# Kernel optimization log

Hardware: AMD Instinct MI355X
Metric: run time of the kernel (lower is better)

Reference implementation:

```python
import jax, jax.numpy as jnp
import numpy as np

L, D, H, EXP = 4, 512, 8, 4
HD = D // H
DFF = D * EXP
B, S = 8, 1024
LN_EPS = 1e-3  # keras LayerNormalization default epsilon


def _glorot(key, shape):
    fan_in, fan_out = shape[-2], shape[-1]
    lim = np.sqrt(6.0 / (fan_in + fan_out))
    return jax.random.uniform(key, shape, jnp.float32, -lim, lim)


def setup_inputs() -> dict:
    key = jax.random.key(0)
    ks = jax.random.split(key, 12)
    x = jax.random.normal(ks[0], (B, S, D), jnp.float32)
    # sequence mask from random lengths (mimics tf.sequence_mask(row_lengths))
    lengths = jax.random.randint(ks[1], (B,), S // 2, S + 1)
    mask = (jnp.arange(S)[None, :] < lengths[:, None])  # [B,S] bool
    inp = {
        'x': x, 'mask': mask,
        'Wq': _glorot(ks[2], (L, D, D)),
        'Wk': _glorot(ks[3], (L, D, D)),
        'Wv': _glorot(ks[4], (L, D, D)),
        'Wo': _glorot(ks[5], (L, D, D)),
        'ln1_g': jnp.ones((L, D), jnp.float32),
        'ln1_b': jnp.zeros((L, D), jnp.float32),
        'ln2_g': jnp.ones((L, D), jnp.float32),
        'ln2_b': jnp.zeros((L, D), jnp.float32),
        'W1': _glorot(ks[6], (L, D, DFF)),
        'b1': jnp.zeros((L, DFF), jnp.float32),
        'W2': _glorot(ks[7], (L, DFF, D)),
        'b2': jnp.zeros((L, D), jnp.float32),
    }
    return inp


def _layernorm(x, g, b):
    mu = jnp.mean(x, axis=-1, keepdims=True)
    var = jnp.mean(jnp.square(x - mu), axis=-1, keepdims=True)
    return (x - mu) * jax.lax.rsqrt(var + LN_EPS) * g + b


def _pos_encoding(s, d):
    # matches the source: sin/cos halves with inv freq 10000**(2j/d), j<d/2
    half = d // 2
    p = jnp.arange(s, dtype=jnp.float32)[:, None]          # [S,1]
    inv = 10000.0 ** (2.0 * jnp.arange(half, dtype=jnp.float32) / d)  # [half]
    ang = p / inv[None, :]                                 # [S,half]
    return jnp.concatenate([jnp.sin(ang), jnp.cos(ang)], axis=1)  # [S,D]


def _forward(x, mask, Wq, Wk, Wv, Wo, ln1_g, ln1_b, ln2_g, ln2_b, W1, b1, W2, b2):
    b, s, d = x.shape
    x = x + _pos_encoding(s, d)
    key_mask = mask[:, None, None, :]  # [B,1,1,Sk]
    scale = 1.0 / jnp.sqrt(jnp.float32(HD))
    for l in range(L):
        h = _layernorm(x, ln1_g[l], ln1_b[l])
        q = (h @ Wq[l]).reshape(b, s, H, HD).transpose(0, 2, 1, 3)  # bhsd
        k = (h @ Wk[l]).reshape(b, s, H, HD).transpose(0, 2, 1, 3)
        v = (h @ Wv[l]).reshape(b, s, H, HD).transpose(0, 2, 1, 3)
        scores = jnp.einsum('bhqd,bhkd->bhqk', q, k) * scale
        scores = jnp.where(key_mask, scores, -1e9)
        attn = jax.nn.softmax(scores, axis=-1)
        o = jnp.einsum('bhqk,bhkd->bhqd', attn, v)
        o = o.transpose(0, 2, 1, 3).reshape(b, s, d) @ Wo[l]
        x = x + o  # dropout rate 0 / inference -> identity
        h = _layernorm(x, ln2_g[l], ln2_b[l])
        f = jax.nn.relu(h @ W1[l] + b1[l]) @ W2[l] + b2[l]
        x = x + f
    return x


def reference(x, mask, Wq, Wk, Wv, Wo, ln1_g, ln1_b, ln2_g, ln2_b, W1, b1, W2, b2):
    return _forward(x, mask, Wq, Wk, Wv, Wo, ln1_g, ln1_b, ln2_g, ln2_b, W1, b1, W2, b2)
```

## Files before the change

### kernel.cpp

```cpp
#include <hip/hip_runtime.h>
#include <math.h>

#define NB 8
#define SEQ 1024
#define DM 512
#define NH 8
#define HDIM 64
#define DFF 2048
#define NLAYER 4
#define NTOK (NB * SEQ)
#define QKVD 1536

typedef __attribute__((ext_vector_type(8))) short bf16x8;
typedef __attribute__((ext_vector_type(4))) float f32x4;

__device__ __forceinline__ ushort f2bf(float f) {
    union { float f; unsigned u; } v; v.f = f;
    unsigned r = (v.u + 0x7FFF + ((v.u >> 16) & 1)) >> 16;
    return (ushort)r;
}

__device__ __forceinline__ void async16(const void* g, void* l) {
    __builtin_amdgcn_global_load_lds(
        (const __attribute__((address_space(1))) unsigned int*)g,
        (__attribute__((address_space(3))) unsigned int*)l, 16, 0, 0);
}

__global__ __launch_bounds__(256) void add_pos_kernel(const float* __restrict__ x,
                                                      float* __restrict__ out) {
    int idx4 = blockIdx.x * blockDim.x + threadIdx.x;
    int base = idx4 * 4;
    int d = base & (DM - 1);
    int s = (base >> 9) & (SEQ - 1);
    float4 v = *(const float4*)&x[base];
    float r[4] = {v.x, v.y, v.z, v.w};
#pragma unroll
    for (int i = 0; i < 4; i++) {
        int dd = d + i;
        float pe;
        if (dd < 256) {
            float inv = powf(10000.0f, 2.0f * (float)dd / 512.0f);
            pe = sinf((float)s / inv);
        } else {
            float inv = powf(10000.0f, 2.0f * (float)(dd - 256) / 512.0f);
            pe = cosf((float)s / inv);
        }
        r[i] += pe;
    }
    *(float4*)&out[base] = make_float4(r[0], r[1], r[2], r[3]);
}

__global__ __launch_bounds__(256) void wtrans_kernel(const float* __restrict__ src,
                                                     ushort* __restrict__ dst,
                                                     int K, int N, int rowOff,
                                                     int layerStride) {
    __shared__ float tile[32][36];
    int l = blockIdx.z;
    int kb = blockIdx.y * 32, nb = blockIdx.x * 32;
    const float* s = src + (size_t)l * K * N;
    ushort* d = dst + (size_t)l * layerStride;
    int r = threadIdx.x >> 3, c4 = (threadIdx.x & 7) * 4;
    float4 v = *(const float4*)&s[(size_t)(kb + r) * N + nb + c4];
    *(float4*)&tile[r][c4] = v;
    __syncthreads();
    ushort4 o;
    o.x = f2bf(tile[c4 + 0][r]);
    o.y = f2bf(tile[c4 + 1][r]);
    o.z = f2bf(tile[c4 + 2][r]);
    o.w = f2bf(tile[c4 + 3][r]);
    *(ushort4*)&d[(size_t)(rowOff + nb + r) * K + kb + c4] = o;
}

__global__ __launch_bounds__(256) void ln_kernel(const float* __restrict__ x,
                                                 const float* __restrict__ g,
                                                 const float* __restrict__ bta,
                                                 ushort* __restrict__ out) {
    int w = threadIdx.x >> 6;
    int lane = threadIdx.x & 63;
    size_t row = (size_t)blockIdx.x * 4 + w;
    const float* xr = x + row * DM;
    float4 v0 = *(const float4*)&xr[lane * 4];
    float4 v1 = *(const float4*)&xr[256 + lane * 4];
    float sum = v0.x + v0.y + v0.z + v0.w + v1.x + v1.y + v1.z + v1.w;
#pragma unroll
    for (int off = 32; off > 0; off >>= 1) sum += __shfl_xor(sum, off, 64);
    float mu = sum * (1.0f / 512.0f);
    float d0[8] = {v0.x - mu, v0.y - mu, v0.z - mu, v0.w - mu,
                   v1.x - mu, v1.y - mu, v1.z - mu, v1.w - mu};
    float sq = 0.0f;
#pragma unroll
    for (int i = 0; i < 8; i++) sq = fmaf(d0[i], d0[i], sq);
#pragma unroll
    for (int off = 32; off > 0; off >>= 1) sq += __shfl_xor(sq, off, 64);
    float rs = rsqrtf(sq * (1.0f / 512.0f) + 1e-3f);
    float4 g0 = *(const float4*)&g[lane * 4];
    float4 g1 = *(const float4*)&g[256 + lane * 4];
    float4 b0 = *(const float4*)&bta[lane * 4];
    float4 b1 = *(const float4*)&bta[256 + lane * 4];
    ushort* orow = out + row * DM;
    ushort4 o0, o1;
    o0.x = f2bf(fmaf(d0[0] * rs, g0.x, b0.x));
    o0.y = f2bf(fmaf(d0[1] * rs, g0.y, b0.y));
    o0.z = f2bf(fmaf(d0[2] * rs, g0.z, b0.z));
    o0.w = f2bf(fmaf(d0[3] * rs, g0.w, b0.w));
    o1.x = f2bf(fmaf(d0[4] * rs, g1.x, b1.x));
    o1.y = f2bf(fmaf(d0[5] * rs, g1.y, b1.y));
    o1.z = f2bf(fmaf(d0[6] * rs, g1.z, b1.z));
    o1.w = f2bf(fmaf(d0[7] * rs, g1.w, b1.w));
    *(ushort4*)&orow[lane * 4] = o0;
    *(ushort4*)&orow[256 + lane * 4] = o1;
}

template <int BM, int BN, int KH, int MODE>
__global__ __launch_bounds__(512) void gemm_bf16(const ushort* __restrict__ A,
                                                 const ushort* __restrict__ Bt,
                                                 const float* __restrict__ bias,
                                                 void* __restrict__ Cv,
                                                 void* __restrict__ aux,
                                                 int M, int N, int K) {
    static_assert(BM % 64 == 0 && BN % 64 == 0, "tile multiple of 64");
    constexpr int FM = BM / 64;
    constexpr int FN = BN / 32;
    __shared__ __align__(16) ushort As[2][KH * BM * 32];
    __shared__ __align__(16) ushort Bs[2][KH * BN * 32];
    const int tid = threadIdx.x;
    const int lane = tid & 63;
    const int w = tid >> 6;

    const int nx = gridDim.x;
    int wg = blockIdx.y * nx + blockIdx.x;
    int xcd = wg & 7;
    int t0 = wg >> 3;
    int bx = t0 % nx;
    int by = (t0 / nx) * 8 + xcd;
    const int m0 = by * BM, n0 = bx * BN;

    const int wm = (w >> 1) * (BM / 4);
    const int wn = (w & 1) * (BN / 2);
    const int fm = lane & 15, fq = lane >> 4;

    f32x4 acc[FM][FN] = {};

    auto stage = [&](int buf, int kt) {
#pragma unroll
        for (int hf = 0; hf < KH; hf++) {
            constexpr int CA = BM * 4;
            if constexpr (CA >= 512) {
#pragma unroll
                for (int u = 0; u < CA / 512; u++) {
                    int chunk = u * 512 + tid;
                    int row = chunk >> 2, c = chunk & 3;
                    async16(&A[(size_t)(m0 + row) * K + kt + hf * 32 + c * 8],
                            (char*)As[buf] + hf * BM * 64 + chunk * 16);
                }
            } else {
                if (tid < CA) {
                    int chunk = tid;
                    int row = chunk >> 2, c = chunk & 3;
                    async16(&A[(size_t)(m0 + row) * K + kt + hf * 32 + c * 8],
                            (char*)As[buf] + hf * BM * 64 + chunk * 16);
                }
            }
            constexpr int CB = BN * 4;
            if constexpr (CB >= 512) {
#pragma unroll
                for (int u = 0; u < CB / 512; u++) {
                    int chunk = u * 512 + tid;
                    int row = chunk >> 2, c = chunk & 3;
                    async16(&Bt[(size_t)(n0 + row) * K + kt + hf * 32 + c * 8],
                            (char*)Bs[buf] + hf * BN * 64 + chunk * 16);
                }
            } else {
                if (tid < CB) {
                    int chunk = tid;
                    int row = chunk >> 2, c = chunk & 3;
                    async16(&Bt[(size_t)(n0 + row) * K + kt + hf * 32 + c * 8],
                            (char*)Bs[buf] + hf * BN * 64 + chunk * 16);
                }
            }
        }
    };

    stage(0, 0);
    __syncthreads();
    int cur = 0;
    for (int kt = 0; kt < K; kt += 32 * KH) {
        if (kt + 32 * KH < K) stage(cur ^ 1, kt + 32 * KH);
#pragma unroll
        for (int hf = 0; hf < KH; hf++) {
            bf16x8 af[FM], bfr[FN];
#pragma unroll
            for (int i = 0; i < FM; i++)
                af[i] = *(const bf16x8*)&As[cur][hf * BM * 32 +
                                                 (wm + i * 16 + fm) * 32 + fq * 8];
#pragma unroll
            for (int j = 0; j < FN; j++)
                bfr[j] = *(const bf16x8*)&Bs[cur][hf * BN * 32 +
                                                  (wn + j * 16 + fm) * 32 + fq * 8];
#pragma unroll
            for (int i = 0; i < FM; i++)
#pragma unroll
                for (int j = 0; j < FN; j++)
                    acc[i][j] = __builtin_amdgcn_mfma_f32_16x16x32_bf16(
                        af[i], bfr[j], acc[i][j], 0, 0, 0);
        }
        __syncthreads();
        cur ^= 1;
    }

    if constexpr (MODE == 5) {
        if (n0 >= 1024) {
            ushort* vT = (ushort*)aux;
            const int b = m0 >> 10;
            const int sl = (m0 & (SEQ - 1)) + wm + fq * 4;
#pragma unroll
            for (int i = 0; i < FM; i++) {
#pragma unroll
                for (int j = 0; j < FN; j++) {
                    int c = n0 - 1024 + wn + j * 16 + fm;
                    ushort4 o;
                    o.x = f2bf(acc[i][j][0]);
                    o.y = f2bf(acc[i][j][1]);
                    o.z = f2bf(acc[i][j][2]);
                    o.w = f2bf(acc[i][j][3]);
                    *(ushort4*)&vT[(size_t)(b * DM + c) * SEQ + sl + i * 16] = o;
                }
            }
        } else {
#pragma unroll
            for (int i = 0; i < FM; i++)
#pragma unroll
                for (int j = 0; j < FN; j++) {
                    int col = n0 + wn + j * 16 + fm;
#pragma unroll
                    for (int r = 0; r < 4; r++) {
                        int row = m0 + wm + i * 16 + fq * 4 + r;
                        ((ushort*)Cv)[(size_t)row * N + col] = f2bf(acc[i][j][r]);
                    }
                }
        }
        return;
    }

#pragma unroll
    for (int i = 0; i < FM; i++) {
#pragma unroll
        for (int j = 0; j < FN; j++) {
            int col = n0 + wn + j * 16 + fm;
#pragma unroll
            for (int r = 0; r < 4; r++) {
                int row = m0 + wm + i * 16 + fq * 4 + r;
                float vv = acc[i][j][r];
                if constexpr (MODE == 0) {
                    ((ushort*)Cv)[(size_t)row * N + col] = f2bf(vv);
                } else if constexpr (MODE == 1) {
                    float* C = (float*)Cv;
                    C[(size_t)row * N + col] += vv;
                } else if constexpr (MODE == 2) {
                    vv += bias[col];
                    vv = fmaxf(vv, 0.0f);
                    ((ushort*)Cv)[(size_t)row * N + col] = f2bf(vv);
                } else {
                    float* C = (float*)Cv;
                    C[(size_t)row * N + col] += vv + bias[col];
                }
            }
        }
    }
}

__global__ __launch_bounds__(512) void attn_mfma(const ushort* __restrict__ QKV,
                                                 const ushort* __restrict__ Vt,
                                                 const int* __restrict__ mask,
                                                 ushort* __restrict__ O) {
    __shared__ __align__(16) ushort Kt[64 * 64];
    __shared__ __align__(16) ushort Vs[64 * 64];
    __shared__ __align__(16) ushort ps[8][16 * 72];
    __shared__ float mskf[64];
    __shared__ int lensh[8];

    const int tid = threadIdx.x, lane = tid & 63, w = tid >> 6;
    const int h = blockIdx.y, b = blockIdx.z;
    const int q0 = blockIdx.x * 128 + w * 16;
    const int fm = lane & 15, fq = lane >> 4;
    ushort* pw = &ps[w][0];
    const float L2E = 1.44269504f;

    int part = mask[b * SEQ + tid] + mask[b * SEQ + 512 + tid];
#pragma unroll
    for (int off = 32; off > 0; off >>= 1) part += __shfl_xor(part, off, 64);
    if (lane == 0) lensh[w] = part;

    bf16x8 qf[2];
#pragma unroll
    for (int kk = 0; kk < 2; kk++) {
        bf16x8 t = *(const bf16x8*)&QKV[(size_t)(b * SEQ + q0 + fm) * QKVD + h * HDIM +
                                        kk * 32 + fq * 8];
#pragma unroll
        for (int j = 0; j < 8; j++) {
            union { float f; unsigned u; } vv;
            vv.u = ((unsigned)(ushort)t[j]) << 16;
            vv.f *= 0.125f;
            t[j] = (short)(ushort)(vv.u >> 16);
        }
        qf[kk] = t;
    }

    const int r0 = tid >> 3, c0 = tid & 7;
    const int dk0 = (r0 * 8 + (c0 ^ (r0 & 7))) * 16;

    auto gK = [&](int j0) {
        return (const uint4*)&QKV[(size_t)(b * SEQ + j0 + r0) * QKVD + 512 +
                                  h * HDIM + c0 * 8];
    };
    auto gV = [&](int j0) {
        return (const uint4*)&Vt[(size_t)((b * NH + h) * HDIM + r0) * SEQ + j0 + c0 * 8];
    };

    uint4 kreg = *gK(0);
    uint4 vreg = *gV(0);
    int mreg = (tid < 64) ? mask[b * SEQ + tid] : 0;
    *(uint4*)((char*)Kt + dk0) = kreg;
    *(uint4*)((char*)Vs + dk0) = vreg;
    if (tid < 64) mskf[tid] = mreg ? 1.0f : 0.0f;
    __syncthreads();

    const int len = lensh[0] + lensh[1] + lensh[2] + lensh[3] +
                    lensh[4] + lensh[5] + lensh[6] + lensh[7];
    const int jmax = (len + 63) & ~63;

    f32x4 oacc[4] = {};
    float mrow = -INFINITY, lrow = 0.0f;

    for (int j0 = 0; j0 < jmax; j0 += 64) {
        const bool has_next = (j0 + 64 < jmax);
        if (has_next) {
            kreg = *gK(j0 + 64);
            vreg = *gV(j0 + 64);
            if (tid < 64) mreg = mask[b * SEQ + j0 + 64 + tid];
        }

        f32x4 sc[4] = {};
        __builtin_amdgcn_s_setprio(1);
#pragma unroll
        for (int nt = 0; nt < 4; nt++) {
            int key = nt * 16 + fm;
#pragma unroll
            for (int kk = 0; kk < 2; kk++) {
                bf16x8 kf = *(const bf16x8*)((char*)Kt +
                            (key * 8 + ((kk * 4 + fq) ^ (key & 7))) * 16);
                sc[nt] = __builtin_amdgcn_mfma_f32_16x16x32_bf16(kf, qf[kk], sc[nt], 0, 0, 0);
            }
        }
        __builtin_amdgcn_s_setprio(0);

        float mx = -INFINITY;
#pragma unroll
        for (int nt = 0; nt < 4; nt++)
#pragma unroll
            for (int r = 0; r < 4; r++) mx = fmaxf(mx, sc[nt][r]);
        mx = fmaxf(mx, __shfl_xor(mx, 16));
        mx = fmaxf(mx, __shfl_xor(mx, 32));
        if (!__all(mx - mrow <= 8.0f)) {
            float mn = fmaxf(mrow, mx);
            float alpha = __expf(mrow - mn);
            mrow = mn;
            lrow *= alpha;
#pragma unroll
            for (int nt = 0; nt < 4; nt++)
#pragma unroll
                for (int r = 0; r < 4; r++) oacc[nt][r] *= alpha;
        }

        const float nm2 = -mrow * L2E;
        float sv[4][4];
        float ls = 0.0f;
#pragma unroll
        for (int nt = 0; nt < 4; nt++) {
            f32x4 mv = *(const f32x4*)&mskf[nt * 16 + fq * 4];
#pragma unroll
            for (int r = 0; r < 4; r++) {
                float p = exp2f(fmaf(sc[nt][r], L2E, nm2)) * mv[r];
                sv[nt][r] = p;
                ls += p;
            }
        }
        ls += __shfl_xor(ls, 16);
        ls += __shfl_xor(ls, 32);
        lrow += ls;

#pragma unroll
        for (int nt = 0; nt < 4; nt++) {
            union { float f; unsigned u; } a0, a1, a2, a3;
            a0.f = sv[nt][0]; a1.f = sv[nt][1]; a2.f = sv[nt][2]; a3.f = sv[nt][3];
            unsigned d0 = (a0.u >> 16) | (a1.u & 0xFFFF0000u);
            unsigned d1 = (a2.u >> 16) | (a3.u & 0xFFFF0000u);
            *(uint2*)&pw[fm * 72 + nt * 16 + fq * 4] = make_uint2(d0, d1);
        }

        __builtin_amdgcn_s_setprio(1);
#pragma unroll
        for (int kk = 0; kk < 2; kk++) {
            bf16x8 pf = *(const bf16x8*)&pw[fm * 72 + kk * 32 + fq * 8];
#pragma unroll
            for (int nt = 0; nt < 4; nt++) {
                int dim = nt * 16 + fm;
                bf16x8 vf = *(const bf16x8*)((char*)Vs +
                            (dim * 8 + ((kk * 4 + fq) ^ (dim & 7))) * 16);
                oacc[nt] = __builtin_amdgcn_mfma_f32_16x16x32_bf16(vf, pf, oacc[nt], 0, 0, 0);
            }
        }
        __builtin_amdgcn_s_setprio(0);

        __syncthreads();
        if (has_next) {
            *(uint4*)((char*)Kt + dk0) = kreg;
            *(uint4*)((char*)Vs + dk0) = vreg;
            if (tid < 64) mskf[tid] = mreg ? 1.0f : 0.0f;
            __syncthreads();
        }
    }

    float inv = 1.0f / lrow;
#pragma unroll
    for (int nt = 0; nt < 4; nt++) {
        ushort4 o;
        o.x = f2bf(oacc[nt][0] * inv);
        o.y = f2bf(oacc[nt][1] * inv);
        o.z = f2bf(oacc[nt][2] * inv);
        o.w = f2bf(oacc[nt][3] * inv);
        *(ushort4*)&O[(size_t)(b * SEQ + q0 + fm) * DM + h * HDIM + nt * 16 + fq * 4] = o;
    }
}

extern "C" void kernel_launch(void* const* d_in, const int* in_sizes, int n_in,
                              void* d_out, int out_size, void* d_ws, size_t ws_size,
                              hipStream_t stream) {
    const float* x_in = (const float*)d_in[0];
    const int* mask   = (const int*)d_in[1];
    const float* Wq   = (const float*)d_in[2];
    const float* Wk   = (const float*)d_in[3];
    const float* Wv   = (const float*)d_in[4];
    const float* Wo   = (const float*)d_in[5];
    const float* ln1g = (const float*)d_in[6];
    const float* ln1b = (const float*)d_in[7];
    const float* ln2g = (const float*)d_in[8];
    const float* ln2b = (const float*)d_in[9];
    const float* W1   = (const float*)d_in[10];
    const float* b1   = (const float*)d_in[11];
    const float* W2   = (const float*)d_in[12];
    const float* b2   = (const float*)d_in[13];

    float* x = (float*)d_out;
    ushort* wsb = (ushort*)d_ws;
    const size_t U = 1048576;
    ushort* WqkvT = wsb;
    ushort* WoT   = wsb + 3 * U;
    ushort* W1T   = wsb + 4 * U;
    ushort* W2T   = wsb + 8 * U;
    ushort* hb    = wsb + 12 * U;
    ushort* qkv   = wsb + 16 * U;
    ushort* ob    = wsb + 28 * U;
    ushort* vTb   = wsb + 32 * U;
    ushort* f1b   = qkv;

    wtrans_kernel<<<dim3(16, 16, 4), 256, 0, stream>>>(Wq, WqkvT, 512, 512, 0, 786432);
    wtrans_kernel<<<dim3(16, 16, 4), 256, 0, stream>>>(Wk, WqkvT, 512, 512, 512, 786432);
    wtrans_kernel<<<dim3(16, 16, 4), 256, 0, stream>>>(Wv, WqkvT, 512, 512, 1024, 786432);
    wtrans_kernel<<<dim3(16, 16, 4), 256, 0, stream>>>(Wo, WoT, 512, 512, 0, 262144);
    wtrans_kernel<<<dim3(64, 16, 4), 256, 0, stream>>>(W1, W1T, 512, 2048, 0, 1048576);
    wtrans_kernel<<<dim3(16, 64, 4), 256, 0, stream>>>(W2, W2T, 2048, 512, 0, 1048576);

    add_pos_kernel<<<(NTOK * DM / 4) / 256, 256, 0, stream>>>(x_in, x);

    dim3 gQKV(QKVD / 64, NTOK / 128);
    dim3 gProj(DM / 64, NTOK / 64);
    dim3 gFF1(DFF / 64, NTOK / 128);
    dim3 gFF2(DM / 64, NTOK / 64);
    dim3 gAttn(SEQ / 128, NH, NB);

    for (int l = 0; l < NLAYER; l++) {
        const size_t wOff   = (size_t)l * 262144;
        const size_t wqkvOff= (size_t)l * 786432;
        const size_t w1Off  = (size_t)l * 1048576;

        ln_kernel<<<NTOK / 4, 256, 0, stream>>>(x, ln1g + l * DM, ln1b + l * DM, hb);
        gemm_bf16<128, 64, 1, 5><<<gQKV, 512, 0, stream>>>(hb, WqkvT + wqkvOff, nullptr,
                                                           qkv, vTb, NTOK, QKVD, DM);
        attn_mfma<<<gAttn, 512, 0, stream>>>(qkv, vTb, mask, ob);
        gemm_bf16<64, 64, 2, 1><<<gProj, 512, 0, stream>>>(ob, WoT + wOff, nullptr, x,
                                                           nullptr, NTOK, DM, DM);
        ln_kernel<<<NTOK / 4, 256, 0, stream>>>(x, ln2g + l * DM, ln2b + l * DM, hb);
        gemm_bf16<128, 64, 1, 2><<<gFF1, 512, 0, stream>>>(hb, W1T + w1Off,
                                                           b1 + (size_t)l * DFF, f1b,
                                                           nullptr, NTOK, DFF, DM);
        gemm_bf16<64, 64, 2, 3><<<gFF2, 512, 0, stream>>>(f1b, W2T + w1Off,
                                                          b2 + (size_t)l * DM, x,
                                                          nullptr, NTOK, DM, DFF);
    }
}
```

Measured before the change: 749.0 us.

## Merge weight transposes into one launch and widen QKV/FF1 GEMM tiles

The six per-matrix weight transpose/convert launches become a single kernel whose flat block index picks the source matrix and tile. The QKV and FF1 GEMMs switch from 128x64 to 128x128 output tiles, halving their grid width. Launch overhead should drop and the larger tiles give more operand reuse per block, at the cost of more registers and LDS per block and fewer blocks to spread across CUs.

```diff
diff --git a/kernel.cpp b/kernel.cpp
--- a/kernel.cpp
+++ b/kernel.cpp
@@ -50,15 +50,35 @@
     *(float4*)&out[base] = make_float4(r[0], r[1], r[2], r[3]);
 }
 
-__global__ __launch_bounds__(256) void wtrans_kernel(const float* __restrict__ src,
-                                                     ushort* __restrict__ dst,
-                                                     int K, int N, int rowOff,
-                                                     int layerStride) {
+__global__ __launch_bounds__(256) void wtrans_all(
+    const float* __restrict__ Wq, const float* __restrict__ Wk,
+    const float* __restrict__ Wv, const float* __restrict__ Wo,
+    const float* __restrict__ W1, const float* __restrict__ W2,
+    ushort* __restrict__ WqkvT, ushort* __restrict__ WoT,
+    ushort* __restrict__ W1T, ushort* __restrict__ W2T) {
     __shared__ float tile[32][36];
-    int l = blockIdx.z;
-    int kb = blockIdx.y * 32, nb = blockIdx.x * 32;
+    const int l = blockIdx.z;
+    const int bid = blockIdx.x;
+    const float* src; ushort* dst;
+    int K, N, rowOff, stride, t, nxk;
+    if (bid < 1024) {
+        int seg = bid >> 8; t = bid & 255;
+        K = 512; N = 512; nxk = 16;
+        if (seg == 0)      { src = Wq; dst = WqkvT; rowOff = 0;    stride = 786432; }
+        else if (seg == 1) { src = Wk; dst = WqkvT; rowOff = 512;  stride = 786432; }
+        else if (seg == 2) { src = Wv; dst = WqkvT; rowOff = 1024; stride = 786432; }
+        else               { src = Wo; dst = WoT;   rowOff = 0;    stride = 262144; }
+    } else if (bid < 2048) {
+        t = bid - 1024; K = 512; N = 2048; nxk = 64;
+        src = W1; dst = W1T; rowOff = 0; stride = 1048576;
+    } else {
+        t = bid - 2048; K = 2048; N = 512; nxk = 16;
+        src = W2; dst = W2T; rowOff = 0; stride = 1048576;
+    }
+    const int bx = t % nxk, by = t / nxk;
+    const int kb = by * 32, nb = bx * 32;
     const float* s = src + (size_t)l * K * N;
-    ushort* d = dst + (size_t)l * layerStride;
+    ushort* d = dst + (size_t)l * stride;
     int r = threadIdx.x >> 3, c4 = (threadIdx.x & 7) * 4;
     float4 v = *(const float4*)&s[(size_t)(kb + r) * N + nb + c4];
     *(float4*)&tile[r][c4] = v;
@@ -464,18 +484,14 @@
     ushort* vTb   = wsb + 32 * U;
     ushort* f1b   = qkv;
 
-    wtrans_kernel<<<dim3(16, 16, 4), 256, 0, stream>>>(Wq, WqkvT, 512, 512, 0, 786432);
-    wtrans_kernel<<<dim3(16, 16, 4), 256, 0, stream>>>(Wk, WqkvT, 512, 512, 512, 786432);
-    wtrans_kernel<<<dim3(16, 16, 4), 256, 0, stream>>>(Wv, WqkvT, 512, 512, 1024, 786432);
-    wtrans_kernel<<<dim3(16, 16, 4), 256, 0, stream>>>(Wo, WoT, 512, 512, 0, 262144);
-    wtrans_kernel<<<dim3(64, 16, 4), 256, 0, stream>>>(W1, W1T, 512, 2048, 0, 1048576);
-    wtrans_kernel<<<dim3(16, 64, 4), 256, 0, stream>>>(W2, W2T, 2048, 512, 0, 1048576);
+    wtrans_all<<<dim3(3072, 1, 4), 256, 0, stream>>>(Wq, Wk, Wv, Wo, W1, W2,
+                                                     WqkvT, WoT, W1T, W2T);
 
     add_pos_kernel<<<(NTOK * DM / 4) / 256, 256, 0, stream>>>(x_in, x);
 
-    dim3 gQKV(QKVD / 64, NTOK / 128);
+    dim3 gQKV(QKVD / 128, NTOK / 128);
     dim3 gProj(DM / 64, NTOK / 64);
-    dim3 gFF1(DFF / 64, NTOK / 128);
+    dim3 gFF1(DFF / 128, NTOK / 128);
     dim3 gFF2(DM / 64, NTOK / 64);
     dim3 gAttn(SEQ / 128, NH, NB);
 
@@ -485,15 +501,15 @@
         const size_t w1Off  = (size_t)l * 1048576;
 
         ln_kernel<<<NTOK / 4, 256, 0, stream>>>(x, ln1g + l * DM, ln1b + l * DM, hb);
-        gemm_bf16<128, 64, 1, 5><<<gQKV, 512, 0, stream>>>(hb, WqkvT + wqkvOff, nullptr,
-                                                           qkv, vTb, NTOK, QKVD, DM);
+        gemm_bf16<128, 128, 1, 5><<<gQKV, 512, 0, stream>>>(hb, WqkvT + wqkvOff, nullptr,
+                                                            qkv, vTb, NTOK, QKVD, DM);
         attn_mfma<<<gAttn, 512, 0, stream>>>(qkv, vTb, mask, ob);
         gemm_bf16<64, 64, 2, 1><<<gProj, 512, 0, stream>>>(ob, WoT + wOff, nullptr, x,
                                                            nullptr, NTOK, DM, DM);
         ln_kernel<<<NTOK / 4, 256, 0, stream>>>(x, ln2g + l * DM, ln2b + l * DM, hb);
-        gemm_bf16<128, 64, 1, 2><<<gFF1, 512, 0, stream>>>(hb, W1T + w1Off,
-                                                           b1 + (size_t)l * DFF, f1b,
-                                                           nullptr, NTOK, DFF, DM);
+        gemm_bf16<128, 128, 1, 2><<<gFF1, 512, 0, stream>>>(hb, W1T + w1Off,
+                                                            b1 + (size_t)l * DFF, f1b,
+                                                            nullptr, NTOK, DFF, DM);
         gemm_bf16<64, 64, 2, 3><<<gFF2, 512, 0, stream>>>(f1b, W2T + w1Off,
                                                           b2 + (size_t)l * DM, x,
                                                           nullptr, NTOK, DM, DFF);
```

Result: faster. 695.8 us (median of 2 runs) (-7.1%).
